# Kernel optimization log

Hardware: AMD Instinct MI355X
Metric: run time of the kernel (lower is better)

## Reference

```python
import jax, jax.numpy as jnp
import numpy as np

B = 2
C = 256          # hidden_dim / d_model
NH = 8           # attention heads
NL = 4           # feature levels
NP = 4           # sampling points per head per level
DH = C // NH
FF = 1024
NLAYERS = 6
SHAPES = [(64, 64), (32, 32), (16, 16), (8, 8)]
CIN = 256
OUT_CH = 2
IMG = 256


def setup_inputs() -> dict:
    key = jax.random.key(0)
    ks = iter(jax.random.split(key, 64))

    def nrm(shape, s=0.02):
        return jax.random.normal(next(ks), shape, jnp.float32) * s

    inp = {}
    for i, (h, w) in enumerate(SHAPES):
        inp[f"f{i}"] = jax.random.normal(next(ks), (B, CIN, h, w), jnp.float32)
    # input_proj: 1x1 conv + GroupNorm per level
    inp["proj_w"] = nrm((NL, C, CIN))
    inp["proj_b"] = jnp.zeros((NL, C), jnp.float32)
    inp["gn_w"] = jnp.ones((NL, C), jnp.float32)
    inp["gn_b"] = jnp.zeros((NL, C), jnp.float32)
    inp["level_embed"] = nrm((NL, C), 1.0)
    # 6 encoder layers (stacked params)
    inp["so_w"] = nrm((NLAYERS, NH * NL * NP * 2, C))   # sampling offsets
    inp["so_b"] = nrm((NLAYERS, NH * NL * NP * 2), 0.1)
    inp["aw_w"] = nrm((NLAYERS, NH * NL * NP, C))       # attention weights
    inp["aw_b"] = jnp.zeros((NLAYERS, NH * NL * NP), jnp.float32)
    inp["vp_w"] = nrm((NLAYERS, C, C))                   # value proj
    inp["vp_b"] = jnp.zeros((NLAYERS, C), jnp.float32)
    inp["op_w"] = nrm((NLAYERS, C, C))                   # output proj
    inp["op_b"] = jnp.zeros((NLAYERS, C), jnp.float32)
    inp["n1_w"] = jnp.ones((NLAYERS, C), jnp.float32)
    inp["n1_b"] = jnp.zeros((NLAYERS, C), jnp.float32)
    inp["l1_w"] = nrm((NLAYERS, FF, C))
    inp["l1_b"] = jnp.zeros((NLAYERS, FF), jnp.float32)
    inp["l2_w"] = nrm((NLAYERS, C, FF))
    inp["l2_b"] = jnp.zeros((NLAYERS, C), jnp.float32)
    inp["n2_w"] = jnp.ones((NLAYERS, C), jnp.float32)
    inp["n2_b"] = jnp.zeros((NLAYERS, C), jnp.float32)
    # classifier head convs
    inp["c1_w"] = nrm((64, C, 3, 3))
    inp["c1_b"] = jnp.zeros((64,), jnp.float32)
    inp["c2_w"] = nrm((OUT_CH, 64, 3, 3))
    inp["c2_b"] = jnp.zeros((OUT_CH,), jnp.float32)
    return inp


def group_norm(x, w, b, groups=32, eps=1e-5):
    Bq, Cc, H, W = x.shape
    xg = x.reshape(Bq, groups, Cc // groups, H, W)
    mu = xg.mean((2, 3, 4), keepdims=True)
    var = xg.var((2, 3, 4), keepdims=True)
    xg = (xg - mu) * jax.lax.rsqrt(var + eps)
    return xg.reshape(Bq, Cc, H, W) * w[None, :, None, None] + b[None, :, None, None]


def layer_norm(x, w, b, eps=1e-5):
    mu = x.mean(-1, keepdims=True)
    var = x.var(-1, keepdims=True)
    return (x - mu) * jax.lax.rsqrt(var + eps) * w + b


def pos_embed_sine(h, w, num_feats=C // 2):
    # PositionEmbeddingSine(normalize=True), mask all-False -> cumsum of ones
    eps = 1e-6
    scale = 2.0 * np.pi
    y = (jnp.arange(1, h + 1, dtype=jnp.float32) / (h + eps)) * scale
    x = (jnp.arange(1, w + 1, dtype=jnp.float32) / (w + eps)) * scale
    dim_t = 10000.0 ** (2.0 * (jnp.arange(num_feats) // 2).astype(jnp.float32) / num_feats)

    def enc(v):
        p = v[:, None] / dim_t  # [n, num_feats]
        return jnp.stack([jnp.sin(p[:, 0::2]), jnp.cos(p[:, 1::2])], -1).reshape(v.shape[0], num_feats)

    pe_y = enc(y)  # [h, 128]
    pe_x = enc(x)  # [w, 128]
    pos = jnp.concatenate([
        jnp.broadcast_to(pe_y[:, None, :], (h, w, num_feats)),
        jnp.broadcast_to(pe_x[None, :, :], (h, w, num_feats)),
    ], -1)  # [h, w, C], channels = (y, x)
    return pos.reshape(h * w, C)


def reference_points(shapes):
    pts = []
    for h, w in shapes:
        ry = (jnp.arange(h, dtype=jnp.float32) + 0.5) / h
        rx = (jnp.arange(w, dtype=jnp.float32) + 0.5) / w
        gy, gx = jnp.meshgrid(ry, rx, indexing='ij')
        pts.append(jnp.stack([gx, gy], -1).reshape(-1, 2))
    return jnp.concatenate(pts, 0)  # [Lq, 2] (x, y)


def bilinear_sample(v, x, y, Hl, Wl):
    # v: [B, NH, S, DH]; x, y: [B, Lq, NH, NP] pixel coords (align_corners=False, zero padding)
    x0 = jnp.floor(x); y0 = jnp.floor(y)
    fx = x - x0; fy = y - y0
    out = 0.0
    for dx, dy, wgt in ((0, 0, (1 - fx) * (1 - fy)), (1, 0, fx * (1 - fy)),
                        (0, 1, (1 - fx) * fy), (1, 1, fx * fy)):
        xi = x0 + dx; yi = y0 + dy
        valid = ((xi >= 0) & (xi < Wl) & (yi >= 0) & (yi < Hl)).astype(v.dtype)
        idx = (jnp.clip(yi, 0, Wl and Hl - 1) * Wl + jnp.clip(xi, 0, Wl - 1)).astype(jnp.int32)
        idx = (jnp.clip(yi, 0, Hl - 1) * Wl + jnp.clip(xi, 0, Wl - 1)).astype(jnp.int32)
        idxh = idx.transpose(0, 2, 1, 3).reshape(idx.shape[0], NH, -1)  # [B,NH,Lq*NP]
        g = jnp.take_along_axis(v, idxh[..., None], axis=2)             # [B,NH,Lq*NP,DH]
        w_ = (wgt * valid).transpose(0, 2, 1, 3).reshape(idx.shape[0], NH, -1, 1)
        out = out + g * w_
    return out  # [B, NH, Lq*NP, DH]


def ms_deform_attn(query, value_in, ref, starts,
                   so_w, so_b, aw_w, aw_b, vp_w, vp_b, op_w, op_b):
    Bq, Lq, _ = query.shape
    value = value_in @ vp_w.T + vp_b                                  # [B, Lin, C]
    value = value.reshape(Bq, -1, NH, DH).transpose(0, 2, 1, 3)       # [B, NH, Lin, DH]
    off = (query @ so_w.T + so_b).reshape(Bq, Lq, NH, NL, NP, 2)
    aw = (query @ aw_w.T + aw_b).reshape(Bq, Lq, NH, NL * NP)
    aw = jax.nn.softmax(aw, -1).reshape(Bq, Lq, NH, NL, NP)
    norm = jnp.array([[w, h] for (h, w) in SHAPES], jnp.float32)       # [NL, 2] (x, y)
    # sampling locations: ref (same across levels, valid_ratios=1) + normalized offsets
    loc = ref[None, :, None, None, None, :] + off / norm[None, None, None, :, None, :]
    out = jnp.zeros((Bq, NH, Lq, DH), jnp.float32)
    for l, (Hl, Wl) in enumerate(SHAPES):
        vl = jax.lax.dynamic_slice_in_dim(value, starts[l], Hl * Wl, axis=2)
        x = loc[:, :, :, l, :, 0] * Wl - 0.5
        y = loc[:, :, :, l, :, 1] * Hl - 0.5
        samp = bilinear_sample(vl, x, y, Hl, Wl).reshape(Bq, NH, Lq, NP, DH)
        out = out + jnp.einsum('bhqp,bhqpd->bhqd', aw[:, :, :, l].transpose(0, 2, 1, 3), samp)
    out = out.transpose(0, 2, 1, 3).reshape(Bq, Lq, C)
    return out @ op_w.T + op_b


def conv3x3(x, w, b):
    y = jax.lax.conv_general_dilated(x, w, (1, 1), ((1, 1), (1, 1)),
                                     dimension_numbers=('NCHW', 'OIHW', 'NCHW'))
    return y + b[None, :, None, None]


def reference(f0, f1, f2, f3, proj_w, proj_b, gn_w, gn_b, level_embed,
              so_w, so_b, aw_w, aw_b, vp_w, vp_b, op_w, op_b,
              n1_w, n1_b, l1_w, l1_b, l2_w, l2_b, n2_w, n2_b,
              c1_w, c1_b, c2_w, c2_b):
    feats = [f0, f1, f2, f3]
    srcs, poss = [], []
    for l, (h, w) in enumerate(SHAPES):
        x = jnp.einsum('oc,bchw->bohw', proj_w[l], feats[l]) + proj_b[l][None, :, None, None]
        x = group_norm(x, gn_w[l], gn_b[l])
        srcs.append(x.reshape(B, C, h * w).transpose(0, 2, 1))   # [B, HW, C]
        poss.append(pos_embed_sine(h, w) + level_embed[l])        # [HW, C]
    src = jnp.concatenate(srcs, 1)       # [B, Lq, C]
    pos = jnp.concatenate(poss, 0)       # [Lq, C]
    ref = reference_points(SHAPES)
    starts = np.cumsum([0] + [h * w for h, w in SHAPES])[:-1].tolist()
    x = src
    for i in range(NLAYERS):  # dropout=0 (eval mode)
        q = x + pos[None]
        a = ms_deform_attn(q, x, ref, starts,
                           so_w[i], so_b[i], aw_w[i], aw_b[i],
                           vp_w[i], vp_b[i], op_w[i], op_b[i])
        x = layer_norm(x + a, n1_w[i], n1_b[i])
        ff = jax.nn.relu(x @ l1_w[i].T + l1_b[i]) @ l2_w[i].T + l2_b[i]
        x = layer_norm(x + ff, n2_w[i], n2_b[i])
    h0, w0 = SHAPES[0]
    layer0 = x[:, :h0 * w0].reshape(B, h0, w0, C).transpose(0, 3, 1, 2)
    y = jax.nn.relu(conv3x3(layer0, c1_w, c1_b))
    y = conv3x3(y, c2_w, c2_b)
    return jax.image.resize(y, (B, OUT_CH, IMG, IMG), method='bilinear')
```

## Files before the change

### kernel.cpp

```cpp
#include <hip/hip_runtime.h>
#include <hip/hip_bf16.h>
#include <math.h>

#define LQ 5440
#define CDIM 256
#define BATCH 2
#define FFDIM 1024

typedef __attribute__((ext_vector_type(8))) short bf16x8;
typedef __attribute__((ext_vector_type(4))) float f32x4;

typedef __attribute__((address_space(1))) void* gas1_t;
typedef __attribute__((address_space(3))) void* las3_t;

__device__ __forceinline__ void async16(const void* g, void* l) {
  __builtin_amdgcn_global_load_lds((gas1_t)g, (las3_t)l, 16, 0, 0);
}

#define WAIT_VM5() asm volatile("s_waitcnt vmcnt(5)" ::: "memory")
#define WAIT_VM4() asm volatile("s_waitcnt vmcnt(4)" ::: "memory")
#define WAIT_VM3() asm volatile("s_waitcnt vmcnt(3)" ::: "memory")
#define WAIT_VM0() asm volatile("s_waitcnt vmcnt(0)" ::: "memory")

__device__ __forceinline__ void get_chunk(int chunk, int& l, int& row0) {
  if (chunk < 64)      { l = 0; row0 = chunk * 64; }
  else if (chunk < 80) { l = 1; row0 = (chunk - 64) * 64; }
  else if (chunk < 84) { l = 2; row0 = (chunk - 80) * 64; }
  else                 { l = 3; row0 = 0; }
}

template <bool RELU, bool OUT_F32, bool OUT_B16, bool REMAP>
__global__ __launch_bounds__(256, 2) void gemm_bf16_kernel(
    const __hip_bfloat16* __restrict__ A, const __hip_bfloat16* __restrict__ Wt,
    const float* __restrict__ bias, float* __restrict__ C,
    __hip_bfloat16* __restrict__ Cb, int M, int N, int K,
    int mrows, long obase, long obstride) {
  __shared__ __hip_bfloat16 As[3][128 * 32];
  __shared__ __hip_bfloat16 Bs[3][128 * 32];
  const int tid = threadIdx.x;
  const int bm = blockIdx.y * 128, bn = blockIdx.x * 128;
  const int lane = tid & 63, wave = tid >> 6;
  const int wr = wave >> 1, wc = wave & 1;
  const int srow = tid >> 2;
  const int scol = (tid & 3) * 8;
  const int lo0 = srow * 32 + scol;
  const int lo1 = (64 + srow) * 32 + scol;
  const __hip_bfloat16* ga0 = A + (size_t)(bm + srow) * K + scol;
  const __hip_bfloat16* ga1 = A + (size_t)(bm + 64 + srow) * K + scol;
  const __hip_bfloat16* gb0 = Wt + (size_t)(bn + srow) * K + scol;
  const __hip_bfloat16* gb1 = Wt + (size_t)(bn + 64 + srow) * K + scol;

  const int nt = K >> 5;
  async16(ga0, &As[0][lo0]);
  async16(ga1, &As[0][lo1]);
  async16(gb0, &Bs[0][lo0]);
  async16(gb1, &Bs[0][lo1]);
  async16(ga0 + 32, &As[1][lo0]);
  async16(ga1 + 32, &As[1][lo1]);
  async16(gb0 + 32, &Bs[1][lo0]);
  async16(gb1 + 32, &Bs[1][lo1]);

  f32x4 acc[4][4] = {};
  const int fr = lane & 15;
  const int ksub = (lane >> 4) * 8;

  int cur = 0, nxt = 2;
  for (int t = 0; t < nt; ++t) {
    if (t == nt - 1) WAIT_VM0(); else WAIT_VM4();
    __builtin_amdgcn_s_barrier();
    asm volatile("" ::: "memory");
    bf16x8 af[4], bfv[4];
    const __hip_bfloat16* as = As[cur];
    const __hip_bfloat16* bs = Bs[cur];
#pragma unroll
    for (int mi = 0; mi < 4; ++mi)
      af[mi] = *(const bf16x8*)&as[(wr * 64 + mi * 16 + fr) * 32 + ksub];
#pragma unroll
    for (int nj = 0; nj < 4; ++nj)
      bfv[nj] = *(const bf16x8*)&bs[(wc * 64 + nj * 16 + fr) * 32 + ksub];
    if (t + 2 < nt) {
      const int ko = (t + 2) * 32;
      async16(ga0 + ko, &As[nxt][lo0]);
      async16(ga1 + ko, &As[nxt][lo1]);
      async16(gb0 + ko, &Bs[nxt][lo0]);
      async16(gb1 + ko, &Bs[nxt][lo1]);
    }
#pragma unroll
    for (int mi = 0; mi < 4; ++mi)
#pragma unroll
      for (int nj = 0; nj < 4; ++nj)
        acc[mi][nj] = __builtin_amdgcn_mfma_f32_16x16x32_bf16(af[mi], bfv[nj],
                                                              acc[mi][nj], 0, 0, 0);
    cur = (cur == 2) ? 0 : cur + 1;
    nxt = (nxt == 2) ? 0 : nxt + 1;
  }

  const int cc = lane & 15;
  const int rbase = (lane >> 4) * 4;
  float bcol[4];
#pragma unroll
  for (int nj = 0; nj < 4; ++nj) bcol[nj] = bias[bn + wc * 64 + nj * 16 + cc];
#pragma unroll
  for (int mi = 0; mi < 4; ++mi)
#pragma unroll
    for (int nj = 0; nj < 4; ++nj) {
      int col = bn + wc * 64 + nj * 16 + cc;
#pragma unroll
      for (int r = 0; r < 4; ++r) {
        int row = bm + wr * 64 + mi * 16 + rbase + r;
        float v = acc[mi][nj][r] + bcol[nj];
        if (RELU) v = fmaxf(v, 0.f);
        if (OUT_F32) {
          size_t oaddr;
          if (REMAP)
            oaddr = (size_t)obase +
                    (row < mrows ? (size_t)row * N
                                 : (size_t)obstride + (size_t)(row - mrows) * N) +
                    col;
          else
            oaddr = (size_t)row * N + col;
          C[oaddr] = v;
        }
        if (OUT_B16) Cb[(size_t)row * N + col] = __float2bfloat16(v);
      }
    }
}

template <bool EMIT_Q>
__global__ __launch_bounds__(256, 2) void gemm_ln_kernel(
    const __hip_bfloat16* __restrict__ A, const __hip_bfloat16* __restrict__ Wt,
    const float* __restrict__ bias, float* __restrict__ x,
    __hip_bfloat16* __restrict__ xb, __hip_bfloat16* __restrict__ qb,
    const float* __restrict__ pos, const float* __restrict__ lnw,
    const float* __restrict__ lnb, int K) {
  __shared__ __hip_bfloat16 As[3][64 * 32];
  __shared__ __hip_bfloat16 Bs[3][256 * 32];
  __shared__ float sred[4][64], ssred[4][64];
  const int tid = threadIdx.x;
  const int bm = blockIdx.x * 64;
  const int lane = tid & 63, wv = tid >> 6;
  const int srow = tid >> 2;
  const int scol = (tid & 3) * 8;
  const int loA = srow * 32 + scol;
  const __hip_bfloat16* ga = A + (size_t)(bm + srow) * K + scol;
  const __hip_bfloat16* gb = Wt + (size_t)srow * K + scol;

  const int nt = K >> 5;
  auto stage = [&](int t, int buf) {
    const int ko = t * 32;
    async16(ga + ko, &As[buf][loA]);
#pragma unroll
    for (int i = 0; i < 4; ++i)
      async16(gb + (size_t)(64 * i) * K + ko, &Bs[buf][(64 * i) * 32 + loA]);
  };
  stage(0, 0);
  stage(1, 1);

  f32x4 acc[4][4] = {};
  const int fr = lane & 15;
  const int ksub = (lane >> 4) * 8;

  int cur = 0, nxt = 2;
  for (int t = 0; t < nt; ++t) {
    if (t == nt - 1) WAIT_VM0(); else WAIT_VM5();
    __builtin_amdgcn_s_barrier();
    asm volatile("" ::: "memory");
    bf16x8 af[4], bfv[4];
#pragma unroll
    for (int mi = 0; mi < 4; ++mi)
      af[mi] = *(const bf16x8*)&As[cur][(mi * 16 + fr) * 32 + ksub];
#pragma unroll
    for (int nj = 0; nj < 4; ++nj)
      bfv[nj] = *(const bf16x8*)&Bs[cur][(wv * 64 + nj * 16 + fr) * 32 + ksub];
    if (t + 2 < nt) stage(t + 2, nxt);
#pragma unroll
    for (int mi = 0; mi < 4; ++mi)
#pragma unroll
      for (int nj = 0; nj < 4; ++nj)
        acc[mi][nj] = __builtin_amdgcn_mfma_f32_16x16x32_bf16(af[mi], bfv[nj],
                                                              acc[mi][nj], 0, 0, 0);
    cur = (cur == 2) ? 0 : cur + 1;
    nxt = (nxt == 2) ? 0 : nxt + 1;
  }

  const int cc = lane & 15;
  const int rbase = (lane >> 4) * 4;
  float bcol[4], wcol[4], bncol[4];
#pragma unroll
  for (int nj = 0; nj < 4; ++nj) {
    int col = wv * 64 + nj * 16 + cc;
    bcol[nj] = bias[col];
    wcol[nj] = lnw[col];
    bncol[nj] = lnb[col];
  }
#pragma unroll
  for (int mi = 0; mi < 4; ++mi)
#pragma unroll
    for (int r = 0; r < 4; ++r) {
      int grow = bm + mi * 16 + rbase + r;
#pragma unroll
      for (int nj = 0; nj < 4; ++nj) {
        int col = wv * 64 + nj * 16 + cc;
        acc[mi][nj][r] += bcol[nj] + x[(size_t)grow * 256 + col];
      }
    }
#pragma unroll
  for (int mi = 0; mi < 4; ++mi)
#pragma unroll
    for (int r = 0; r < 4; ++r) {
      float s = 0.f, ssq = 0.f;
#pragma unroll
      for (int nj = 0; nj < 4; ++nj) {
        float v = acc[mi][nj][r];
        s += v;
        ssq += v * v;
      }
#pragma unroll
      for (int m = 1; m < 16; m <<= 1) {
        s += __shfl_xor(s, m);
        ssq += __shfl_xor(ssq, m);
      }
      if (cc == 0) {
        int row = mi * 16 + rbase + r;
        sred[wv][row] = s;
        ssred[wv][row] = ssq;
      }
    }
  __syncthreads();
#pragma unroll
  for (int mi = 0; mi < 4; ++mi)
#pragma unroll
    for (int r = 0; r < 4; ++r) {
      int row = mi * 16 + rbase + r;
      int grow = bm + row;
      float s = sred[0][row] + sred[1][row] + sred[2][row] + sred[3][row];
      float ssq = ssred[0][row] + ssred[1][row] + ssred[2][row] + ssred[3][row];
      float mu = s * (1.0f / 256.0f);
      float var = ssq * (1.0f / 256.0f) - mu * mu;
      float rsig = rsqrtf(var + 1e-5f);
      int tokp = grow >= LQ ? grow - LQ : grow;
#pragma unroll
      for (int nj = 0; nj < 4; ++nj) {
        int col = wv * 64 + nj * 16 + cc;
        float xn = (acc[mi][nj][r] - mu) * rsig * wcol[nj] + bncol[nj];
        x[(size_t)grow * 256 + col] = xn;
        xb[(size_t)grow * 256 + col] = __float2bfloat16(xn);
        if (EMIT_Q)
          qb[(size_t)grow * 256 + col] =
              __float2bfloat16(xn + pos[(size_t)tokp * 256 + col]);
      }
    }
}

__global__ __launch_bounds__(256, 2) void conv1_mfma_kernel(
    const __hip_bfloat16* __restrict__ xb, const __hip_bfloat16* __restrict__ wc1,
    const float* __restrict__ bias, const __hip_bfloat16* __restrict__ zerob,
    __hip_bfloat16* __restrict__ c1o) {
  __shared__ __hip_bfloat16 As[3][128 * 32];
  __shared__ __hip_bfloat16 Bs[3][64 * 32];
  const int tid = threadIdx.x;
  const int b = blockIdx.x >> 5;
  const int pm = (blockIdx.x & 31) * 128;
  const int lane = tid & 63, wave = tid >> 6;
  const int sr = tid >> 2;
  const int sc = (tid & 3) * 8;
  const int loA0 = sr * 32 + sc, loA1 = (64 + sr) * 32 + sc;
  f32x4 acc[2][4] = {};
  const int fr = lane & 15, ksub = (lane >> 4) * 8;

  auto stage = [&](int kt, int buf) {
    int tap = kt >> 3;
    int kk = (kt & 7) * 32;
    int dy = tap / 3 - 1, dx = tap % 3 - 1;
    int hw0 = pm + sr;
    int y0 = (hw0 >> 6) + dy, x0 = (hw0 & 63) + dx;
    bool ok0 = (y0 >= 0 && y0 < 64 && x0 >= 0 && x0 < 64);
    const __hip_bfloat16* s0 =
        xb + ((size_t)(b * LQ) + y0 * 64 + x0) * 256 + kk + sc;
    int hw1 = pm + 64 + sr;
    int y1 = (hw1 >> 6) + dy, x1 = (hw1 & 63) + dx;
    bool ok1 = (y1 >= 0 && y1 < 64 && x1 >= 0 && x1 < 64);
    const __hip_bfloat16* s1 =
        xb + ((size_t)(b * LQ) + y1 * 64 + x1) * 256 + kk + sc;
    const __hip_bfloat16* wsrc = wc1 + (size_t)sr * 2304 + tap * 256 + kk + sc;
    async16(ok0 ? s0 : zerob, &As[buf][loA0]);
    async16(ok1 ? s1 : zerob, &As[buf][loA1]);
    async16(wsrc, &Bs[buf][loA0]);
  };
  stage(0, 0);
  stage(1, 1);
  int cur = 0, nxt = 2;
  for (int kt = 0; kt < 72; ++kt) {
    if (kt == 71) WAIT_VM0(); else WAIT_VM3();
    __builtin_amdgcn_s_barrier();
    asm volatile("" ::: "memory");
    bf16x8 af[2], bfv[4];
#pragma unroll
    for (int mi = 0; mi < 2; ++mi)
      af[mi] = *(const bf16x8*)&As[cur][(wave * 32 + mi * 16 + fr) * 32 + ksub];
#pragma unroll
    for (int nj = 0; nj < 4; ++nj)
      bfv[nj] = *(const bf16x8*)&Bs[cur][(nj * 16 + fr) * 32 + ksub];
    if (kt + 2 < 72) stage(kt + 2, nxt);
#pragma unroll
    for (int mi = 0; mi < 2; ++mi)
#pragma unroll
      for (int nj = 0; nj < 4; ++nj)
        acc[mi][nj] = __builtin_amdgcn_mfma_f32_16x16x32_bf16(
            af[mi], bfv[nj], acc[mi][nj], 0, 0, 0);
    cur = (cur == 2) ? 0 : cur + 1;
    nxt = (nxt == 2) ? 0 : nxt + 1;
  }
  const int cc = lane & 15;
  const int rbase = (lane >> 4) * 4;
#pragma unroll
  for (int mi = 0; mi < 2; ++mi)
#pragma unroll
    for (int nj = 0; nj < 4; ++nj) {
      int col = nj * 16 + cc;
      float bb = bias[col];
#pragma unroll
      for (int r = 0; r < 4; ++r) {
        int row = wave * 32 + mi * 16 + rbase + r;
        float v = fmaxf(acc[mi][nj][r] + bb, 0.f);
        c1o[(size_t)(b * 4096 + pm + row) * 64 + col] = __float2bfloat16(v);
      }
    }
}

__global__ void f2b_multi_kernel(const float* __restrict__ p0, const float* __restrict__ p1,
                                 const float* __restrict__ p2, const float* __restrict__ p3,
                                 const float* __restrict__ p4,
                                 __hip_bfloat16* __restrict__ o0, __hip_bfloat16* __restrict__ o1,
                                 __hip_bfloat16* __restrict__ o2, __hip_bfloat16* __restrict__ o3,
                                 __hip_bfloat16* __restrict__ o4) {
  int i = blockIdx.x * 256 + threadIdx.x;
  if (i >= 1048576) return;
  const float* in;
  __hip_bfloat16* out;
  int j;
  if (i < 65536)       { in = p0; out = o0; j = i; }
  else if (i < 163840) { in = p1; out = o1; j = i - 65536; }
  else if (i < 262144) { in = p2; out = o2; j = i - 163840; }
  else if (i < 655360) { in = p3; out = o3; j = i - 262144; }
  else                 { in = p4; out = o4; j = i - 655360; }
  float4 v = ((const float4*)in)[j];
  union { ushort4 u; __hip_bfloat16 h[4]; } p;
  p.h[0] = __float2bfloat16(v.x);
  p.h[1] = __float2bfloat16(v.y);
  p.h[2] = __float2bfloat16(v.z);
  p.h[3] = __float2bfloat16(v.w);
  ((ushort4*)out)[j] = p.u;
}

__global__ void sowa_prep_kernel(const float* __restrict__ so_w,
                                 const float* __restrict__ aw_w,
                                 const float* __restrict__ so_b,
                                 const float* __restrict__ aw_b,
                                 __hip_bfloat16* __restrict__ out,
                                 float* __restrict__ bias_out) {
  int i = blockIdx.x * 256 + threadIdx.x;
  if (i < 6 * 384 * 256) {
    int il = i / (384 * 256);
    int rem = i - il * 384 * 256;
    int n = rem >> 8, k = rem & 255;
    float v = (n < 256) ? so_w[(size_t)il * 65536 + n * 256 + k]
                        : aw_w[(size_t)il * 32768 + (n - 256) * 256 + k];
    out[i] = __float2bfloat16(v);
  } else if (i < 6 * 384 * 256 + 6 * 384) {
    int j = i - 6 * 384 * 256;
    int il = j / 384, n = j % 384;
    bias_out[j] = (n < 256) ? so_b[il * 256 + n] : aw_b[il * 128 + n - 256];
  }
}

__global__ void wc1_prep_kernel(const float* __restrict__ w,
                                __hip_bfloat16* __restrict__ out) {
  int i = blockIdx.x * 256 + threadIdx.x;
  if (i >= 64 * 2304) return;
  int oc = i / 2304, r = i % 2304;
// ... 100 lines not shown
__global__ void gn_apply_kernel(float* __restrict__ x, __hip_bfloat16* __restrict__ xb,
                                __hip_bfloat16* __restrict__ qb,
                                const float* __restrict__ pos,
                                const float2* __restrict__ stats,
                                const float* __restrict__ gw, const float* __restrict__ gb) {
  int idx = blockIdx.x * 256 + threadIdx.x;
  if (idx >= BATCH * LQ * CDIM) return;
  int c = idx & 255;
  int tok = idx >> 8;
  int b = tok / LQ, t = tok % LQ;
  int l, hw, Hl, Wl;
  get_level(t, l, hw, Hl, Wl);
  float2 st = stats[(b * 4 + l) * 32 + (c >> 3)];
  float v = (x[idx] - st.x) * st.y * gw[l * CDIM + c] + gb[l * CDIM + c];
  x[idx] = v;
  xb[idx] = __float2bfloat16(v);
  qb[idx] = __float2bfloat16(v + pos[t * 256 + c]);
}

__global__ void pos_embed_kernel(const float* __restrict__ level_embed,
                                 float* __restrict__ pos) {
  int idx = blockIdx.x * 256 + threadIdx.x;
  if (idx >= LQ * CDIM) return;
  int t = idx >> 8, c = idx & 255;
  int l, hw, Hl, Wl;
  get_level(t, l, hw, Hl, Wl);
  int y = hw / Wl, xx = hw % Wl;
  const float twopi = 6.28318530717958647692f;
  float v; int cc;
  if (c < 128) { v = (float)(y + 1) * twopi / ((float)Hl + 1e-6f); cc = c; }
  else         { v = (float)(xx + 1) * twopi / ((float)Wl + 1e-6f); cc = c - 128; }
  int k = cc >> 1;
  float dim_t = expf((float)k * (logf(10000.0f) / 64.0f));
  float p = v / dim_t;
  float e = (cc & 1) ? cosf(p) : sinf(p);
  pos[idx] = e + level_embed[l * CDIM + c];
}

__global__ void ref_kernel(float* __restrict__ ref) {
  int t = blockIdx.x * 256 + threadIdx.x;
  if (t >= LQ) return;
  int l, hw, Hl, Wl;
  get_level(t, l, hw, Hl, Wl);
  int y = hw / Wl, xx = hw % Wl;
  ref[t * 2]     = ((float)xx + 0.5f) / (float)Wl;
  ref[t * 2 + 1] = ((float)y + 0.5f) / (float)Hl;
}

__global__ __launch_bounds__(256) void deform_attn_kernel(
    const __hip_bfloat16* __restrict__ value, const float* __restrict__ comb,
    const float* __restrict__ ref, __hip_bfloat16* __restrict__ out) {
  const int Wl_[4] = {64, 32, 16, 8};
  const int st_[4] = {0, 4096, 5120, 5376};
  int gid = blockIdx.x * 32 + (threadIdx.x >> 3);
  int lane8 = threadIdx.x & 7;
  int h = gid & 7;
  int tok = gid >> 3;
  int b = tok / LQ;
  int qi = tok - b * LQ;

  const float4* awv = (const float4*)(comb + (size_t)tok * 384 + 256 + h * 16);
  float4 q0 = awv[0], q1 = awv[1], q2 = awv[2], q3 = awv[3];
  float logit[16] = {q0.x, q0.y, q0.z, q0.w, q1.x, q1.y, q1.z, q1.w,
                     q2.x, q2.y, q2.z, q2.w, q3.x, q3.y, q3.z, q3.w};
  float mx = -1e30f;
#pragma unroll
  for (int i = 0; i < 16; ++i) mx = fmaxf(mx, logit[i]);
  const float LOG2E = 1.4426950408889634f;
  float ssum = 0.f;
#pragma unroll
  for (int i = 0; i < 16; ++i) {
    logit[i] = exp2f((logit[i] - mx) * LOG2E);
    ssum += logit[i];
  }
  float inv = 1.0f / ssum;

  float rx = ref[qi * 2], ry = ref[qi * 2 + 1];
  const float4* offv = (const float4*)(comb + (size_t)tok * 384 + h * 32);
  float acc0 = 0.f, acc1 = 0.f, acc2 = 0.f, acc3 = 0.f;

#pragma unroll
  for (int l = 0; l < 4; ++l) {
    const int Wl = Wl_[l];
    const float fW = (float)Wl;
    const __hip_bfloat16* vbase =
        value + ((size_t)b * LQ + st_[l]) * CDIM + h * 32 + lane8 * 4;
    float bx = fmaf(rx, fW, -0.5f);
    float by = fmaf(ry, fW, -0.5f);
    float4 oa = offv[l * 2], ob = offv[l * 2 + 1];
    float oxs[4] = {oa.x, oa.z, ob.x, ob.z};
    float oys[4] = {oa.y, oa.w, ob.y, ob.w};
#pragma unroll
    for (int p = 0; p < 4; ++p) {
      float px = bx + oxs[p], py = by + oys[p];
      float wgt = logit[l * 4 + p] * inv;
      float fpx = floorf(px), fpy = floorf(py);
      int x0 = (int)fpx, y0 = (int)fpy;
      float fx = px - fpx, fy = py - fpy;
      float wx0 = (x0 >= 0 && x0 < Wl) ? (1.f - fx) : 0.f;
      float wx1 = (x0 >= -1 && x0 < Wl - 1) ? fx : 0.f;
      float wy0 = (y0 >= 0 && y0 < Wl) ? (wgt * (1.f - fy)) : 0.f;
      float wy1 = (y0 >= -1 && y0 < Wl - 1) ? (wgt * fy) : 0.f;
      int xc0 = min(max(x0, 0), Wl - 1);
      int xc1 = min(max(x0 + 1, 0), Wl - 1);
      int yc0 = min(max(y0, 0), Wl - 1);
      int yc1 = min(max(y0 + 1, 0), Wl - 1);
      const __hip_bfloat16* r0 = vbase + (size_t)(yc0 * Wl) * CDIM;
      const __hip_bfloat16* r1 = vbase + (size_t)(yc1 * Wl) * CDIM;
      ushort4 u00 = *(const ushort4*)(r0 + (size_t)xc0 * CDIM);
      ushort4 u01 = *(const ushort4*)(r0 + (size_t)xc1 * CDIM);
      ushort4 u10 = *(const ushort4*)(r1 + (size_t)xc0 * CDIM);
      ushort4 u11 = *(const ushort4*)(r1 + (size_t)xc1 * CDIM);
      float w00 = wy0 * wx0, w01 = wy0 * wx1, w10 = wy1 * wx0, w11 = wy1 * wx1;
      acc0 = fmaf(w00, __uint_as_float((unsigned)u00.x << 16), acc0);
      acc1 = fmaf(w00, __uint_as_float((unsigned)u00.y << 16), acc1);
      acc2 = fmaf(w00, __uint_as_float((unsigned)u00.z << 16), acc2);
      acc3 = fmaf(w00, __uint_as_float((unsigned)u00.w << 16), acc3);
      acc0 = fmaf(w01, __uint_as_float((unsigned)u01.x << 16), acc0);
      acc1 = fmaf(w01, __uint_as_float((unsigned)u01.y << 16), acc1);
      acc2 = fmaf(w01, __uint_as_float((unsigned)u01.z << 16), acc2);
      acc3 = fmaf(w01, __uint_as_float((unsigned)u01.w << 16), acc3);
      acc0 = fmaf(w10, __uint_as_float((unsigned)u10.x << 16), acc0);
      acc1 = fmaf(w10, __uint_as_float((unsigned)u10.y << 16), acc1);
      acc2 = fmaf(w10, __uint_as_float((unsigned)u10.z << 16), acc2);
      acc3 = fmaf(w10, __uint_as_float((unsigned)u10.w << 16), acc3);
      acc0 = fmaf(w11, __uint_as_float((unsigned)u11.x << 16), acc0);
      acc1 = fmaf(w11, __uint_as_float((unsigned)u11.y << 16), acc1);
      acc2 = fmaf(w11, __uint_as_float((unsigned)u11.z << 16), acc2);
      acc3 = fmaf(w11, __uint_as_float((unsigned)u11.w << 16), acc3);
    }
  }
  union { ushort4 u; __hip_bfloat16 hh[4]; } pk;
  pk.hh[0] = __float2bfloat16(acc0);
  pk.hh[1] = __float2bfloat16(acc1);
  pk.hh[2] = __float2bfloat16(acc2);
  pk.hh[3] = __float2bfloat16(acc3);
  *(ushort4*)(out + (size_t)tok * CDIM + h * 32 + lane8 * 4) = pk.u;
}

__global__ __launch_bounds__(256) void conv2_part_kernel(
    const __hip_bfloat16* __restrict__ c1o, const float* __restrict__ w,
    float* __restrict__ part) {
  int pix = blockIdx.x * 256 + threadIdx.x;
  int tap = blockIdx.y, b = blockIdx.z;
  int y = pix >> 6, x = pix & 63;
  int dy = tap / 3 - 1, dx = tap % 3 - 1;
  int yy = y + dy, xx = x + dx;
  bool ok = (yy >= 0 && yy < 64 && xx >= 0 && xx < 64);
  float a0 = 0.f, a1 = 0.f;
  if (ok) {
    const __hip_bfloat16* row = c1o + (size_t)(b * 4096 + yy * 64 + xx) * 64;
#pragma unroll
    for (int ic4 = 0; ic4 < 16; ++ic4) {
      ushort4 u = *(const ushort4*)(row + ic4 * 4);
      float f0 = __uint_as_float((unsigned)u.x << 16);
      float f1 = __uint_as_float((unsigned)u.y << 16);
      float f2 = __uint_as_float((unsigned)u.z << 16);
      float f3 = __uint_as_float((unsigned)u.w << 16);
      int ic = ic4 * 4;
      a0 = fmaf(w[(ic + 0) * 9 + tap], f0, a0);
      a0 = fmaf(w[(ic + 1) * 9 + tap], f1, a0);
      a0 = fmaf(w[(ic + 2) * 9 + tap], f2, a0);
      a0 = fmaf(w[(ic + 3) * 9 + tap], f3, a0);
      a1 = fmaf(w[576 + (ic + 0) * 9 + tap], f0, a1);
      a1 = fmaf(w[576 + (ic + 1) * 9 + tap], f1, a1);
      a1 = fmaf(w[576 + (ic + 2) * 9 + tap], f2, a1);
      a1 = fmaf(w[576 + (ic + 3) * 9 + tap], f3, a1);
    }
  }
  float2 o = make_float2(a0, a1);
  *(float2*)&part[((size_t)(tap * BATCH + b) * 4096 + pix) * 2] = o;
}

__global__ void conv2_reduce_kernel(const float* __restrict__ part,
                                    const float* __restrict__ bias,
                                    float* __restrict__ out) {
  int i = blockIdx.x * 256 + threadIdx.x;
  if (i >= BATCH * 4096) return;
  int b = i >> 12, pix = i & 4095;
  float s0 = bias[0], s1 = bias[1];
#pragma unroll
  for (int tap = 0; tap < 9; ++tap) {
    float2 v = *(const float2*)&part[((size_t)(tap * BATCH + b) * 4096 + pix) * 2];
    s0 += v.x; s1 += v.y;
  }
  *(float2*)&out[(size_t)i * 2] = make_float2(s0, s1);
}

__global__ void upsample_kernel(const float* __restrict__ in, float* __restrict__ out) {
  int idx = blockIdx.x * 256 + threadIdx.x;
// ... 64 lines not shown
  __hip_bfloat16* ff1b = (__hip_bfloat16*)(ws + o);  o += (size_t)BATCH * LQ * FFDIM / 2;
  __hip_bfloat16* sowa_wb = (__hip_bfloat16*)(ws + o); o += 294912;
  __hip_bfloat16* vp_wb = (__hip_bfloat16*)(ws + o); o += 196608;
  __hip_bfloat16* op_wb = (__hip_bfloat16*)(ws + o); o += 196608;
  __hip_bfloat16* l1_wb = (__hip_bfloat16*)(ws + o); o += 786432;
  __hip_bfloat16* l2_wb = (__hip_bfloat16*)(ws + o); o += 786432;
  __hip_bfloat16* proj_wb = (__hip_bfloat16*)(ws + o); o += 131072;
  __hip_bfloat16* wc1b = (__hip_bfloat16*)(ws + o);  o += 73728;
  __hip_bfloat16* c1ob = ff1b;
  float* part2 = (float*)(ff1b + 524288);
  float* c2o = part2 + 147456;

  const int HWs[4] = {4096, 1024, 256, 64};
  const int STs[4] = {0, 4096, 5120, 5376};

  hipMemsetAsync(zerof, 0, 1024, stream);
  sowa_prep_kernel<<<(6 * 384 * 256 + 6 * 384 + 255) / 256, 256, 0, stream>>>(
      so_w, aw_w, so_b, aw_b, sowa_wb, sowa_bias);
  wc1_prep_kernel<<<(147456 + 255) / 256, 256, 0, stream>>>(c1_w, wc1b);
  f2b_multi_kernel<<<(1048576 + 255) / 256, 256, 0, stream>>>(
      proj_w, vp_w, op_w, l1_w, l2_w, proj_wb, vp_wb, op_wb, l1_wb, l2_wb);

  transpose_f_kernel<<<dim3(85, 4, BATCH), 256, 0, stream>>>(f[0], f[1], f[2], f[3],
                                                             ftb);
  for (int l = 0; l < 4; ++l) {
    int M2 = 2 * HWs[l];
    gemm_bf16_kernel<false, true, false, true><<<dim3(2, M2 / 128), 256, 0, stream>>>(
        ftb + (size_t)2 * STs[l] * 256, proj_wb + (size_t)l * 65536,
        proj_b + (size_t)l * 256, x, nullptr, M2, 256, 256,
        HWs[l], (long)STs[l] * 256, (long)LQ * 256);
  }
  pos_embed_kernel<<<(LQ * CDIM + 255) / 256, 256, 0, stream>>>(level_embed, pos);
  ref_kernel<<<(LQ + 255) / 256, 256, 0, stream>>>(refb);
  gn_part_kernel<<<dim3(85, BATCH), 256, 0, stream>>>(x, gnpart);
  gn_finalize_kernel<<<1, 256, 0, stream>>>(gnpart, stats);
  {
    int n = BATCH * LQ * CDIM;
    gn_apply_kernel<<<(n + 255) / 256, 256, 0, stream>>>(x, xb, qb, pos, stats,
                                                         gn_w, gn_b);
  }

  const int M = BATCH * LQ;
  for (int i = 0; i < 6; ++i) {
    const __hip_bfloat16* sowa = sowa_wb + (size_t)i * 98304;
    const __hip_bfloat16* vw = vp_wb + (size_t)i * 65536;
    const __hip_bfloat16* ow = op_wb + (size_t)i * 65536;
    const __hip_bfloat16* w1 = l1_wb + (size_t)i * 262144;
    const __hip_bfloat16* w2 = l2_wb + (size_t)i * 262144;
    const float* vb = vp_b + (size_t)i * CDIM;
    const float* ob = op_b + (size_t)i * CDIM;
    const float* b1 = l1_b + (size_t)i * FFDIM;
    const float* b2 = l2_b + (size_t)i * CDIM;

    gemm_bf16_kernel<false, false, true, false><<<dim3(2, 85), 256, 0, stream>>>(
        xb, vw, vb, nullptr, valb, M, CDIM, CDIM, 0, 0, 0);
    gemm_bf16_kernel<false, true, false, false><<<dim3(3, 85), 256, 0, stream>>>(
        qb, sowa, sowa_bias + i * 384, comb, nullptr, M, 384, CDIM, 0, 0, 0);
    deform_attn_kernel<<<BATCH * LQ * 8 / 32, 256, 0, stream>>>(valb, comb, refb,
                                                                attnb);
    gemm_ln_kernel<false><<<170, 256, 0, stream>>>(
        attnb, ow, ob, x, xb, nullptr, nullptr,
        n1_w + (size_t)i * CDIM, n1_b + (size_t)i * CDIM, CDIM);
    gemm_bf16_kernel<true, false, true, false><<<dim3(8, 85), 256, 0, stream>>>(
        xb, w1, b1, nullptr, ff1b, M, FFDIM, CDIM, 0, 0, 0);
    gemm_ln_kernel<true><<<170, 256, 0, stream>>>(
        ff1b, w2, b2, x, xb, qb, pos,
        n2_w + (size_t)i * CDIM, n2_b + (size_t)i * CDIM, FFDIM);
  }

  conv1_mfma_kernel<<<64, 256, 0, stream>>>(xb, wc1b, c1_b,
                                            (const __hip_bfloat16*)zerof, c1ob);
  conv2_part_kernel<<<dim3(16, 9, BATCH), 256, 0, stream>>>(c1ob, c2_w, part2);
  conv2_reduce_kernel<<<(BATCH * 4096 + 255) / 256, 256, 0, stream>>>(part2, c2_b,
                                                                      c2o);
  {
    int n = BATCH * 2 * 256 * 256;
    upsample_kernel<<<(n + 255) / 256, 256, 0, stream>>>(c2o, (float*)d_out);
  }
}
```

Measured before the change: 715.2 us.

## Merge value/offset GEMMs, shrink tiles for more blocks, widen deform-attn loads

The value-projection and sampling-offset GEMMs become one launch of 850 blocks using a 64x128 tile with higher occupancy. The LayerNorm-fused GEMMs and the conv1 kernel switch to half-height tiles, doubling the block count so more of the GPU's compute units stay busy. The deformable attention kernel now gives each thread 8 channels with 16-byte loads and stores, using 4 threads per head instead of 8. These changes target under-filled grids and launch overhead, at the cost of less weight-tile reuse per block.

```diff
diff --git a/kernel.cpp b/kernel.cpp
--- a/kernel.cpp
+++ b/kernel.cpp
@@ -20,6 +20,7 @@
 #define WAIT_VM5() asm volatile("s_waitcnt vmcnt(5)" ::: "memory")
 #define WAIT_VM4() asm volatile("s_waitcnt vmcnt(4)" ::: "memory")
 #define WAIT_VM3() asm volatile("s_waitcnt vmcnt(3)" ::: "memory")
+#define WAIT_VM2() asm volatile("s_waitcnt vmcnt(2)" ::: "memory")
 #define WAIT_VM0() asm volatile("s_waitcnt vmcnt(0)" ::: "memory")
 
 __device__ __forceinline__ void get_chunk(int chunk, int& l, int& row0) {
@@ -126,6 +127,93 @@
     }
 }
 
+template <bool OUT_F32, bool OUT_B16>
+__device__ __forceinline__ void gemm64_body(
+    const __hip_bfloat16* __restrict__ A, const __hip_bfloat16* __restrict__ Wt,
+    const float* __restrict__ bias, float* __restrict__ C,
+    __hip_bfloat16* __restrict__ Cb, int bm, int bn, int N, int K,
+    __hip_bfloat16 (*As)[64 * 32], __hip_bfloat16 (*Bs)[128 * 32]) {
+  const int tid = threadIdx.x;
+  const int lane = tid & 63, wv = tid >> 6;
+  const int srow = tid >> 2, scol = (tid & 3) * 8;
+  const int loA = srow * 32 + scol;
+  const int loB1 = (64 + srow) * 32 + scol;
+  const __hip_bfloat16* ga = A + (size_t)(bm + srow) * K + scol;
+  const __hip_bfloat16* gb0 = Wt + (size_t)(bn + srow) * K + scol;
+  const __hip_bfloat16* gb1 = Wt + (size_t)(bn + 64 + srow) * K + scol;
+  const int nt = K >> 5;
+  async16(ga, &As[0][loA]);
+  async16(gb0, &Bs[0][loA]);
+  async16(gb1, &Bs[0][loB1]);
+  async16(ga + 32, &As[1][loA]);
+  async16(gb0 + 32, &Bs[1][loA]);
+  async16(gb1 + 32, &Bs[1][loB1]);
+
+  f32x4 acc[4][2] = {};
+  const int fr = lane & 15, ksub = (lane >> 4) * 8;
+  int cur = 0, nxt = 2;
+  for (int t = 0; t < nt; ++t) {
+    if (t == nt - 1) WAIT_VM0(); else WAIT_VM3();
+    __builtin_amdgcn_s_barrier();
+    asm volatile("" ::: "memory");
+    bf16x8 af[4], bfv[2];
+#pragma unroll
+    for (int mi = 0; mi < 4; ++mi)
+      af[mi] = *(const bf16x8*)&As[cur][(mi * 16 + fr) * 32 + ksub];
+#pragma unroll
+    for (int nj = 0; nj < 2; ++nj)
+      bfv[nj] = *(const bf16x8*)&Bs[cur][(wv * 32 + nj * 16 + fr) * 32 + ksub];
+    if (t + 2 < nt) {
+      const int ko = (t + 2) * 32;
+      async16(ga + ko, &As[nxt][loA]);
+      async16(gb0 + ko, &Bs[nxt][loA]);
+      async16(gb1 + ko, &Bs[nxt][loB1]);
+    }
+#pragma unroll
+    for (int mi = 0; mi < 4; ++mi)
+#pragma unroll
+      for (int nj = 0; nj < 2; ++nj)
+        acc[mi][nj] = __builtin_amdgcn_mfma_f32_16x16x32_bf16(af[mi], bfv[nj],
+                                                              acc[mi][nj], 0, 0, 0);
+    cur = (cur == 2) ? 0 : cur + 1;
+    nxt = (nxt == 2) ? 0 : nxt + 1;
+  }
+  const int cc = lane & 15;
+  const int rbase = (lane >> 4) * 4;
+#pragma unroll
+  for (int nj = 0; nj < 2; ++nj) {
+    int col = bn + wv * 32 + nj * 16 + cc;
+    float bb = bias[col];
+#pragma unroll
+    for (int mi = 0; mi < 4; ++mi)
+#pragma unroll
+      for (int r = 0; r < 4; ++r) {
+        int row = bm + mi * 16 + rbase + r;
+        float v = acc[mi][nj][r] + bb;
+        if (OUT_F32) C[(size_t)row * N + col] = v;
+        if (OUT_B16) Cb[(size_t)row * N + col] = __float2bfloat16(v);
+      }
+  }
+}
+
+__global__ __launch_bounds__(256, 4) void gemm_dual_kernel(
+    const __hip_bfloat16* __restrict__ xb, const __hip_bfloat16* __restrict__ vw,
+    const float* __restrict__ vb, __hip_bfloat16* __restrict__ valb,
+    const __hip_bfloat16* __restrict__ qb, const __hip_bfloat16* __restrict__ sowa,
+    const float* __restrict__ sbias, float* __restrict__ comb) {
+  __shared__ __hip_bfloat16 As[3][64 * 32];
+  __shared__ __hip_bfloat16 Bs[3][128 * 32];
+  if (blockIdx.x < 340) {
+    int i = blockIdx.x;
+    gemm64_body<false, true>(xb, vw, vb, nullptr, valb, (i >> 1) * 64,
+                             (i & 1) * 128, 256, 256, As, Bs);
+  } else {
+    int j = blockIdx.x - 340;
+    gemm64_body<true, false>(qb, sowa, sbias, comb, nullptr, (j / 3) * 64,
+                             (j % 3) * 128, 384, 256, As, Bs);
+  }
+}
+
 template <bool EMIT_Q>
 __global__ __launch_bounds__(256, 2) void gemm_ln_kernel(
     const __hip_bfloat16* __restrict__ A, const __hip_bfloat16* __restrict__ Wt,
@@ -133,16 +221,17 @@
     __hip_bfloat16* __restrict__ xb, __hip_bfloat16* __restrict__ qb,
     const float* __restrict__ pos, const float* __restrict__ lnw,
     const float* __restrict__ lnb, int K) {
-  __shared__ __hip_bfloat16 As[3][64 * 32];
+  __shared__ __hip_bfloat16 As[3][32 * 32];
   __shared__ __hip_bfloat16 Bs[3][256 * 32];
-  __shared__ float sred[4][64], ssred[4][64];
+  __shared__ float sred[4][32], ssred[4][32];
   const int tid = threadIdx.x;
-  const int bm = blockIdx.x * 64;
+  const int bm = blockIdx.x * 32;
   const int lane = tid & 63, wv = tid >> 6;
   const int srow = tid >> 2;
+  const int arow = srow & 31;
   const int scol = (tid & 3) * 8;
-  const int loA = srow * 32 + scol;
-  const __hip_bfloat16* ga = A + (size_t)(bm + srow) * K + scol;
+  const int loA = arow * 32 + scol;
+  const __hip_bfloat16* ga = A + (size_t)(bm + arow) * K + scol;
   const __hip_bfloat16* gb = Wt + (size_t)srow * K + scol;
 
   const int nt = K >> 5;
@@ -151,12 +240,12 @@
     async16(ga + ko, &As[buf][loA]);
 #pragma unroll
     for (int i = 0; i < 4; ++i)
-      async16(gb + (size_t)(64 * i) * K + ko, &Bs[buf][(64 * i) * 32 + loA]);
+      async16(gb + (size_t)(64 * i) * K + ko, &Bs[buf][(64 * i + srow) * 32 + scol]);
   };
   stage(0, 0);
   stage(1, 1);
 
-  f32x4 acc[4][4] = {};
+  f32x4 acc[2][4] = {};
   const int fr = lane & 15;
   const int ksub = (lane >> 4) * 8;
 
@@ -165,16 +254,16 @@
     if (t == nt - 1) WAIT_VM0(); else WAIT_VM5();
     __builtin_amdgcn_s_barrier();
     asm volatile("" ::: "memory");
-    bf16x8 af[4], bfv[4];
-#pragma unroll
-    for (int mi = 0; mi < 4; ++mi)
+    bf16x8 af[2], bfv[4];
+#pragma unroll
+    for (int mi = 0; mi < 2; ++mi)
       af[mi] = *(const bf16x8*)&As[cur][(mi * 16 + fr) * 32 + ksub];
 #pragma unroll
     for (int nj = 0; nj < 4; ++nj)
       bfv[nj] = *(const bf16x8*)&Bs[cur][(wv * 64 + nj * 16 + fr) * 32 + ksub];
     if (t + 2 < nt) stage(t + 2, nxt);
 #pragma unroll
-    for (int mi = 0; mi < 4; ++mi)
+    for (int mi = 0; mi < 2; ++mi)
 #pragma unroll
       for (int nj = 0; nj < 4; ++nj)
         acc[mi][nj] = __builtin_amdgcn_mfma_f32_16x16x32_bf16(af[mi], bfv[nj],
@@ -194,7 +283,7 @@
     bncol[nj] = lnb[col];
   }
 #pragma unroll
-  for (int mi = 0; mi < 4; ++mi)
+  for (int mi = 0; mi < 2; ++mi)
 #pragma unroll
     for (int r = 0; r < 4; ++r) {
       int grow = bm + mi * 16 + rbase + r;
@@ -205,7 +294,7 @@
       }
     }
 #pragma unroll
-  for (int mi = 0; mi < 4; ++mi)
+  for (int mi = 0; mi < 2; ++mi)
 #pragma unroll
     for (int r = 0; r < 4; ++r) {
       float s = 0.f, ssq = 0.f;
@@ -228,7 +317,7 @@
     }
   __syncthreads();
 #pragma unroll
-  for (int mi = 0; mi < 4; ++mi)
+  for (int mi = 0; mi < 2; ++mi)
 #pragma unroll
     for (int r = 0; r < 4; ++r) {
       int row = mi * 16 + rbase + r;
@@ -252,80 +341,68 @@
     }
 }
 
-__global__ __launch_bounds__(256, 2) void conv1_mfma_kernel(
+__global__ __launch_bounds__(256, 4) void conv1_mfma_kernel(
     const __hip_bfloat16* __restrict__ xb, const __hip_bfloat16* __restrict__ wc1,
     const float* __restrict__ bias, const __hip_bfloat16* __restrict__ zerob,
     __hip_bfloat16* __restrict__ c1o) {
-  __shared__ __hip_bfloat16 As[3][128 * 32];
+  __shared__ __hip_bfloat16 As[3][64 * 32];
   __shared__ __hip_bfloat16 Bs[3][64 * 32];
   const int tid = threadIdx.x;
-  const int b = blockIdx.x >> 5;
-  const int pm = (blockIdx.x & 31) * 128;
+  const int b = blockIdx.x >> 6;
+  const int pm = (blockIdx.x & 63) * 64;
   const int lane = tid & 63, wave = tid >> 6;
   const int sr = tid >> 2;
   const int sc = (tid & 3) * 8;
-  const int loA0 = sr * 32 + sc, loA1 = (64 + sr) * 32 + sc;
-  f32x4 acc[2][4] = {};
+  const int lo = sr * 32 + sc;
+  f32x4 acc[4] = {};
   const int fr = lane & 15, ksub = (lane >> 4) * 8;
 
   auto stage = [&](int kt, int buf) {
     int tap = kt >> 3;
     int kk = (kt & 7) * 32;
     int dy = tap / 3 - 1, dx = tap % 3 - 1;
-    int hw0 = pm + sr;
-    int y0 = (hw0 >> 6) + dy, x0 = (hw0 & 63) + dx;
-    bool ok0 = (y0 >= 0 && y0 < 64 && x0 >= 0 && x0 < 64);
-    const __hip_bfloat16* s0 =
-        xb + ((size_t)(b * LQ) + y0 * 64 + x0) * 256 + kk + sc;
-    int hw1 = pm + 64 + sr;
-    int y1 = (hw1 >> 6) + dy, x1 = (hw1 & 63) + dx;
-    bool ok1 = (y1 >= 0 && y1 < 64 && x1 >= 0 && x1 < 64);
-    const __hip_bfloat16* s1 =
-        xb + ((size_t)(b * LQ) + y1 * 64 + x1) * 256 + kk + sc;
+    int hw = pm + sr;
+    int y = (hw >> 6) + dy, x = (hw & 63) + dx;
+    bool ok = (y >= 0 && y < 64 && x >= 0 && x < 64);
+    const __hip_bfloat16* s =
+        xb + ((size_t)(b * LQ) + y * 64 + x) * 256 + kk + sc;
     const __hip_bfloat16* wsrc = wc1 + (size_t)sr * 2304 + tap * 256 + kk + sc;
-    async16(ok0 ? s0 : zerob, &As[buf][loA0]);
-    async16(ok1 ? s1 : zerob, &As[buf][loA1]);
-    async16(wsrc, &Bs[buf][loA0]);
+    async16(ok ? s : zerob, &As[buf][lo]);
+    async16(wsrc, &Bs[buf][lo]);
   };
   stage(0, 0);
   stage(1, 1);
   int cur = 0, nxt = 2;
   for (int kt = 0; kt < 72; ++kt) {
-    if (kt == 71) WAIT_VM0(); else WAIT_VM3();
+    if (kt == 71) WAIT_VM0(); else WAIT_VM2();
     __builtin_amdgcn_s_barrier();
     asm volatile("" ::: "memory");
-    bf16x8 af[2], bfv[4];
-#pragma unroll
-    for (int mi = 0; mi < 2; ++mi)
-      af[mi] = *(const bf16x8*)&As[cur][(wave * 32 + mi * 16 + fr) * 32 + ksub];
+    bf16x8 af;
+    bf16x8 bfv[4];
+    af = *(const bf16x8*)&As[cur][(wave * 16 + fr) * 32 + ksub];
 #pragma unroll
     for (int nj = 0; nj < 4; ++nj)
       bfv[nj] = *(const bf16x8*)&Bs[cur][(nj * 16 + fr) * 32 + ksub];
     if (kt + 2 < 72) stage(kt + 2, nxt);
 #pragma unroll
-    for (int mi = 0; mi < 2; ++mi)
-#pragma unroll
-      for (int nj = 0; nj < 4; ++nj)
-        acc[mi][nj] = __builtin_amdgcn_mfma_f32_16x16x32_bf16(
-            af[mi], bfv[nj], acc[mi][nj], 0, 0, 0);
+    for (int nj = 0; nj < 4; ++nj)
+      acc[nj] = __builtin_amdgcn_mfma_f32_16x16x32_bf16(af, bfv[nj], acc[nj], 0, 0, 0);
     cur = (cur == 2) ? 0 : cur + 1;
     nxt = (nxt == 2) ? 0 : nxt + 1;
   }
   const int cc = lane & 15;
   const int rbase = (lane >> 4) * 4;
 #pragma unroll
-  for (int mi = 0; mi < 2; ++mi)
-#pragma unroll
-    for (int nj = 0; nj < 4; ++nj) {
-      int col = nj * 16 + cc;
-      float bb = bias[col];
-#pragma unroll
-      for (int r = 0; r < 4; ++r) {
-        int row = wave * 32 + mi * 16 + rbase + r;
-        float v = fmaxf(acc[mi][nj][r] + bb, 0.f);
-        c1o[(size_t)(b * 4096 + pm + row) * 64 + col] = __float2bfloat16(v);
-      }
+  for (int nj = 0; nj < 4; ++nj) {
+    int col = nj * 16 + cc;
+    float bb = bias[col];
+#pragma unroll
+    for (int r = 0; r < 4; ++r) {
+      int row = wave * 16 + rbase + r;
+      float v = fmaxf(acc[nj][r] + bb, 0.f);
+      c1o[(size_t)(b * 4096 + pm + row) * 64 + col] = __float2bfloat16(v);
     }
+  }
 }
 
 __global__ void f2b_multi_kernel(const float* __restrict__ p0, const float* __restrict__ p1,
@@ -532,8 +609,8 @@
     const float* __restrict__ ref, __hip_bfloat16* __restrict__ out) {
   const int Wl_[4] = {64, 32, 16, 8};
   const int st_[4] = {0, 4096, 5120, 5376};
-  int gid = blockIdx.x * 32 + (threadIdx.x >> 3);
-  int lane8 = threadIdx.x & 7;
+  int gid = blockIdx.x * 64 + (threadIdx.x >> 2);
+  int lane4 = threadIdx.x & 3;
   int h = gid & 7;
   int tok = gid >> 3;
   int b = tok / LQ;
@@ -557,14 +634,14 @@
 
   float rx = ref[qi * 2], ry = ref[qi * 2 + 1];
   const float4* offv = (const float4*)(comb + (size_t)tok * 384 + h * 32);
-  float acc0 = 0.f, acc1 = 0.f, acc2 = 0.f, acc3 = 0.f;
+  float acc[8] = {};
 
 #pragma unroll
   for (int l = 0; l < 4; ++l) {
     const int Wl = Wl_[l];
     const float fW = (float)Wl;
     const __hip_bfloat16* vbase =
-        value + ((size_t)b * LQ + st_[l]) * CDIM + h * 32 + lane8 * 4;
+        value + ((size_t)b * LQ + st_[l]) * CDIM + h * 32 + lane4 * 8;
     float bx = fmaf(rx, fW, -0.5f);
     float by = fmaf(ry, fW, -0.5f);
     float4 oa = offv[l * 2], ob = offv[l * 2 + 1];
@@ -587,35 +664,28 @@
       int yc1 = min(max(y0 + 1, 0), Wl - 1);
       const __hip_bfloat16* r0 = vbase + (size_t)(yc0 * Wl) * CDIM;
       const __hip_bfloat16* r1 = vbase + (size_t)(yc1 * Wl) * CDIM;
-      ushort4 u00 = *(const ushort4*)(r0 + (size_t)xc0 * CDIM);
-      ushort4 u01 = *(const ushort4*)(r0 + (size_t)xc1 * CDIM);
-      ushort4 u10 = *(const ushort4*)(r1 + (size_t)xc0 * CDIM);
-      ushort4 u11 = *(const ushort4*)(r1 + (size_t)xc1 * CDIM);
+      bf16x8 u00 = *(const bf16x8*)(r0 + (size_t)xc0 * CDIM);
+      bf16x8 u01 = *(const bf16x8*)(r0 + (size_t)xc1 * CDIM);
+      bf16x8 u10 = *(const bf16x8*)(r1 + (size_t)xc0 * CDIM);
+      bf16x8 u11 = *(const bf16x8*)(r1 + (size_t)xc1 * CDIM);
       float w00 = wy0 * wx0, w01 = wy0 * wx1, w10 = wy1 * wx0, w11 = wy1 * wx1;
-      acc0 = fmaf(w00, __uint_as_float((unsigned)u00.x << 16), acc0);
-      acc1 = fmaf(w00, __uint_as_float((unsigned)u00.y << 16), acc1);
-      acc2 = fmaf(w00, __uint_as_float((unsigned)u00.z << 16), acc2);
-      acc3 = fmaf(w00, __uint_as_float((unsigned)u00.w << 16), acc3);
-      acc0 = fmaf(w01, __uint_as_float((unsigned)u01.x << 16), acc0);
-      acc1 = fmaf(w01, __uint_as_float((unsigned)u01.y << 16), acc1);
-      acc2 = fmaf(w01, __uint_as_float((unsigned)u01.z << 16), acc2);
-      acc3 = fmaf(w01, __uint_as_float((unsigned)u01.w << 16), acc3);
-      acc0 = fmaf(w10, __uint_as_float((unsigned)u10.x << 16), acc0);
-      acc1 = fmaf(w10, __uint_as_float((unsigned)u10.y << 16), acc1);
-      acc2 = fmaf(w10, __uint_as_float((unsigned)u10.z << 16), acc2);
-      acc3 = fmaf(w10, __uint_as_float((unsigned)u10.w << 16), acc3);
-      acc0 = fmaf(w11, __uint_as_float((unsigned)u11.x << 16), acc0);
-      acc1 = fmaf(w11, __uint_as_float((unsigned)u11.y << 16), acc1);
-      acc2 = fmaf(w11, __uint_as_float((unsigned)u11.z << 16), acc2);
-      acc3 = fmaf(w11, __uint_as_float((unsigned)u11.w << 16), acc3);
+#pragma unroll
+      for (int k = 0; k < 8; ++k) {
+        float v00 = __uint_as_float((unsigned)(unsigned short)u00[k] << 16);
+        float v01 = __uint_as_float((unsigned)(unsigned short)u01[k] << 16);
+        float v10 = __uint_as_float((unsigned)(unsigned short)u10[k] << 16);
+        float v11 = __uint_as_float((unsigned)(unsigned short)u11[k] << 16);
+        acc[k] = fmaf(w00, v00, acc[k]);
+        acc[k] = fmaf(w01, v01, acc[k]);
+        acc[k] = fmaf(w10, v10, acc[k]);
+        acc[k] = fmaf(w11, v11, acc[k]);
+      }
     }
   }
-  union { ushort4 u; __hip_bfloat16 hh[4]; } pk;
-  pk.hh[0] = __float2bfloat16(acc0);
-  pk.hh[1] = __float2bfloat16(acc1);
-  pk.hh[2] = __float2bfloat16(acc2);
-  pk.hh[3] = __float2bfloat16(acc3);
-  *(ushort4*)(out + (size_t)tok * CDIM + h * 32 + lane8 * 4) = pk.u;
+  union { bf16x8 u; __hip_bfloat16 hh[8]; } pk;
+#pragma unroll
+  for (int k = 0; k < 8; ++k) pk.hh[k] = __float2bfloat16(acc[k]);
+  *(bf16x8*)(out + (size_t)tok * CDIM + h * 32 + lane4 * 8) = pk.u;
 }
 
 __global__ __launch_bounds__(256) void conv2_part_kernel(
@@ -786,24 +856,22 @@
     const float* b1 = l1_b + (size_t)i * FFDIM;
     const float* b2 = l2_b + (size_t)i * CDIM;
 
-    gemm_bf16_kernel<false, false, true, false><<<dim3(2, 85), 256, 0, stream>>>(
-        xb, vw, vb, nullptr, valb, M, CDIM, CDIM, 0, 0, 0);
-    gemm_bf16_kernel<false, true, false, false><<<dim3(3, 85), 256, 0, stream>>>(
-        qb, sowa, sowa_bias + i * 384, comb, nullptr, M, 384, CDIM, 0, 0, 0);
-    deform_attn_kernel<<<BATCH * LQ * 8 / 32, 256, 0, stream>>>(valb, comb, refb,
+    gemm_dual_kernel<<<850, 256, 0, stream>>>(xb, vw, vb, valb, qb, sowa,
+                                              sowa_bias + i * 384, comb);
+    deform_attn_kernel<<<BATCH * LQ * 8 / 64, 256, 0, stream>>>(valb, comb, refb,
                                                                 attnb);
-    gemm_ln_kernel<false><<<170, 256, 0, stream>>>(
+    gemm_ln_kernel<false><<<340, 256, 0, stream>>>(
         attnb, ow, ob, x, xb, nullptr, nullptr,
         n1_w + (size_t)i * CDIM, n1_b + (size_t)i * CDIM, CDIM);
     gemm_bf16_kernel<true, false, true, false><<<dim3(8, 85), 256, 0, stream>>>(
         xb, w1, b1, nullptr, ff1b, M, FFDIM, CDIM, 0, 0, 0);
-    gemm_ln_kernel<true><<<170, 256, 0, stream>>>(
+    gemm_ln_kernel<true><<<340, 256, 0, stream>>>(
         ff1b, w2, b2, x, xb, qb, pos,
         n2_w + (size_t)i * CDIM, n2_b + (size_t)i * CDIM, FFDIM);
   }
 
-  conv1_mfma_kernel<<<64, 256, 0, stream>>>(xb, wc1b, c1_b,
-                                            (const __hip_bfloat16*)zerof, c1ob);
+  conv1_mfma_kernel<<<128, 256, 0, stream>>>(xb, wc1b, c1_b,
+                                             (const __hip_bfloat16*)zerof, c1ob);
   conv2_part_kernel<<<dim3(16, 9, BATCH), 256, 0, stream>>>(c1ob, c2_w, part2);
   conv2_reduce_kernel<<<(BATCH * 4096 + 255) / 256, 256, 0, stream>>>(part2, c2_b,
                                                                       c2o);
```

After: 636.8 us. 11.0% less time.
